# Kernel tuning notes

Measured on AMD Instinct MI355X. Metric: run time of the kernel, lower is better.

The kernel has to match this reference:

```python
import jax, jax.numpy as jnp
import numpy as np

E, T, A, H = 64, 128, 32, 4
S, O, QH1, QD, C1 = 256, 128, 128, 64, 128  # state, obs, query hidden, query/key dim, c hidden


def setup_inputs() -> dict:
    key = jax.random.key(0)
    ks = jax.random.split(key, 10)
    w = 0.02
    return {
        "q_values": jax.random.normal(ks[0], (E, T, A), jnp.float32),
        "states": jax.random.normal(ks[1], (E, T, S), jnp.float32),
        "individual_fs": jax.random.normal(ks[2], (E, T, A, O), jnp.float32),
        "Wq1": jax.random.normal(ks[3], (S, QH1), jnp.float32) * w,
        "bq1": jnp.zeros((QH1,), jnp.float32),
        "Wq2": jax.random.normal(ks[4], (QH1, QD), jnp.float32) * w,
        "bq2": jnp.zeros((QD,), jnp.float32),
        "Wk": jax.random.normal(ks[5], (H, O, QD), jnp.float32) * w,
        "bk": jnp.zeros((H, QD), jnp.float32),
        "Wc1": jax.random.normal(ks[6], (S, C1), jnp.float32) * w,
        "bc1": jnp.zeros((C1,), jnp.float32),
        "Wc2": jax.random.normal(ks[7], (C1, 1), jnp.float32) * w,
        "bc2": jnp.zeros((1,), jnp.float32),
    }


def reference(q_values, states, individual_fs, Wq1, bq1, Wq2, bq2, Wk, bk, Wc1, bc1, Wc2, bc2):
    e, t, a = q_values.shape
    s = states.reshape(-1, states.shape[-1])              # (B, S), B = E*T
    f = individual_fs.reshape(e * t, a, -1)               # (B, A, O)
    # query embedding of state: 2-layer MLP with ReLU
    emb_s = jnp.maximum(s @ Wq1 + bq1, 0.0) @ Wq2 + bq2   # (B, QD)
    # all-agents, all-heads key extraction in one batched einsum
    emb_u = jnp.einsum('bao,hok->bahk', f, Wk) + bk       # (B, A, H, QD)
    # query-key dot products per agent/head, then sum over heads
    Lambda_i = jnp.einsum('bk,bahk->bah', emb_s, emb_u).sum(axis=-1)  # (B, A)
    # state-dependent scalar bias
    c_value = jnp.maximum(s @ Wc1 + bc1, 0.0) @ Wc2 + bc2  # (B, 1)
    Q_tot = jnp.sum(Lambda_i * q_values.reshape(-1, a), axis=-1, keepdims=True) + c_value
    return Q_tot.reshape(e, t, 1)
```

## Files before the change

kernel.cpp:

```cpp
#include <hip/hip_runtime.h>


static constexpr int Sd  = 256;
static constexpr int Ad  = 32;
static constexpr int Od  = 128;
static constexpr int QDd = 64;
static constexpr int NB  = 8;
static constexpr int A_BLOCKS = 1024;
static constexpr int B_BLOCKS = 2048;

__global__ void qatten_prep(const float* __restrict__ Wk, const float* __restrict__ bk,
                            float* __restrict__ WkT, float* __restrict__ bkSum)
{
    int idx = blockIdx.x * 256 + threadIdx.x;
    int k = idx >> 7;
    int o = idx & 127;
    float s = 0.f;
#pragma unroll
    for (int h = 0; h < 4; ++h) s += Wk[h * (Od * QDd) + o * QDd + k];
    WkT[k * Od + o] = s;
    if (idx < QDd) {
        float t = 0.f;
#pragma unroll
        for (int h = 0; h < 4; ++h) t += bk[h * QDd + idx];
        bkSum[idx] = t;
    }
}

__global__ __launch_bounds__(256, 6) void qatten_main(
    const float* __restrict__ qv, const float* __restrict__ st, const float* __restrict__ fs,
    const float* __restrict__ Wq1, const float* __restrict__ bq1,
    const float* __restrict__ Wq2, const float* __restrict__ bq2,
    const float* __restrict__ Wc1, const float* __restrict__ bc1,
    const float* __restrict__ Wc2, const float* __restrict__ bc2,
    const float* __restrict__ WkT, const float* __restrict__ bkSum,
    float* __restrict__ v_out, float* __restrict__ bias_out, float* __restrict__ g_out)
{
    __shared__ float s_lds[NB][Sd];
    __shared__ float h_lds[NB][260];
    __shared__ float emb_lds[NB][QDd];

    const int tid = threadIdx.x;

    if (blockIdx.x < A_BLOCKS) {
        const int b0 = blockIdx.x * NB;

        {
            const float4* sp = (const float4*)(st + (size_t)b0 * Sd);
            float4* sl = (float4*)&s_lds[0][0];
            sl[tid] = sp[tid];
            sl[tid + 256] = sp[tid + 256];
        }
        __syncthreads();

        {
            const float* W  = (tid < 128) ? (Wq1 + tid) : (Wc1 + (tid - 128));
            const float  bb = (tid < 128) ? bq1[tid] : bc1[tid - 128];
            float acc[NB];
#pragma unroll
            for (int r = 0; r < NB; ++r) acc[r] = 0.f;
#pragma unroll 4
            for (int i = 0; i < Sd; i += 4) {
                const float w0 = W[(size_t)(i + 0) * 128];
                const float w1 = W[(size_t)(i + 1) * 128];
                const float w2 = W[(size_t)(i + 2) * 128];
                const float w3 = W[(size_t)(i + 3) * 128];
#pragma unroll
                for (int r = 0; r < NB; ++r) {
                    const float4 sv = *(const float4*)&s_lds[r][i];
                    float a = acc[r];
                    a = fmaf(sv.x, w0, a);
                    a = fmaf(sv.y, w1, a);
                    a = fmaf(sv.z, w2, a);
                    a = fmaf(sv.w, w3, a);
                    acc[r] = a;
                }
            }
#pragma unroll
            for (int r = 0; r < NB; ++r)
                h_lds[r][tid] = fmaxf(acc[r] + bb, 0.f);
        }
        __syncthreads();

        {
            const int k = tid & 63;
            const int rg = tid >> 6;
            float a0 = 0.f, a1 = 0.f;
#pragma unroll 4
            for (int j = 0; j < 128; j += 4) {
                const float w0 = Wq2[(size_t)(j + 0) * 64 + k];
                const float w1 = Wq2[(size_t)(j + 1) * 64 + k];
                const float w2 = Wq2[(size_t)(j + 2) * 64 + k];
                const float w3 = Wq2[(size_t)(j + 3) * 64 + k];
                const float4 h0 = *(const float4*)&h_lds[rg][j];
                const float4 h1 = *(const float4*)&h_lds[rg + 4][j];
                a0 = fmaf(h0.x, w0, a0);  a1 = fmaf(h1.x, w0, a1);
                a0 = fmaf(h0.y, w1, a0);  a1 = fmaf(h1.y, w1, a1);
                a0 = fmaf(h0.z, w2, a0);  a1 = fmaf(h1.z, w2, a1);
                a0 = fmaf(h0.w, w3, a0);  a1 = fmaf(h1.w, w3, a1);
            }
            const float bias = bq2[k];
            emb_lds[rg][k] = a0 + bias;
            emb_lds[rg + 4][k] = a1 + bias;
        }
        __syncthreads();

        {
            const int o = tid & 127;
            const int rg = (tid >> 7) * 4;
            float acc[4] = {0.f, 0.f, 0.f, 0.f};
#pragma unroll 4
            for (int k = 0; k < QDd; k += 4) {
                const float w0 = WkT[(size_t)(k + 0) * 128 + o];
                const float w1 = WkT[(size_t)(k + 1) * 128 + o];
                const float w2 = WkT[(size_t)(k + 2) * 128 + o];
                const float w3 = WkT[(size_t)(k + 3) * 128 + o];
#pragma unroll
                for (int r = 0; r < 4; ++r) {
                    const float4 ev = *(const float4*)&emb_lds[rg + r][k];
                    float a = acc[r];
                    a = fmaf(ev.x, w0, a);
                    a = fmaf(ev.y, w1, a);
                    a = fmaf(ev.z, w2, a);
                    a = fmaf(ev.w, w3, a);
                    acc[r] = a;
                }
            }
#pragma unroll
            for (int r = 0; r < 4; ++r)
                v_out[(size_t)(b0 + rg + r) * Od + o] = acc[r];
        }

        {
            const int b = tid >> 5;
            const int i = tid & 31;
            float pb = 0.f, pc = 0.f;
#pragma unroll
            for (int k = i; k < QDd; k += 32)  pb = fmaf(emb_lds[b][k], bkSum[k], pb);
#pragma unroll
            for (int j = i; j < 128; j += 32)  pc = fmaf(h_lds[b][128 + j], Wc2[j], pc);
            float pq = qv[(size_t)b0 * Ad + tid];
#pragma unroll
            for (int d = 16; d >= 1; d >>= 1) {
                pb += __shfl_down(pb, d, 32);
                pc += __shfl_down(pc, d, 32);
                pq += __shfl_down(pq, d, 32);
            }
            if (i == 0) bias_out[b0 + b] = (pc + bc2[0]) + pb * pq;
        }
    } else {
        const int bb = ((int)blockIdx.x - A_BLOCKS) * 4 + (tid >> 6);
        const int l  = tid & 63;
        const float4* __restrict__ fb = (const float4*)fs + (size_t)bb * (Ad * Od / 4);
        const float qreg = qv[(size_t)bb * Ad + (l & 31)];
        float4 acc = {0.f, 0.f, 0.f, 0.f};
#pragma unroll
        for (int i = 0; i < 16; ++i) {
            const float4 f4 = fb[i * 64 + l];
            const float  qa = __shfl(qreg, 2 * i + (l >> 5), 64);
            acc.x = fmaf(qa, f4.x, acc.x);
            acc.y = fmaf(qa, f4.y, acc.y);
            acc.z = fmaf(qa, f4.z, acc.z);
            acc.w = fmaf(qa, f4.w, acc.w);
        }
        acc.x += __shfl_xor(acc.x, 32, 64);
        acc.y += __shfl_xor(acc.y, 32, 64);
        acc.z += __shfl_xor(acc.z, 32, 64);
        acc.w += __shfl_xor(acc.w, 32, 64);
        if (l < 32)
            *(float4*)(g_out + (size_t)bb * Od + l * 4) = acc;
    }
}

__global__ __launch_bounds__(256, 8) void qatten_final(
    const float* __restrict__ g, const float* __restrict__ v,
    const float* __restrict__ bias, float* __restrict__ out)
{
    const int tid = threadIdx.x;
    const int b = blockIdx.x * 8 + (tid >> 5);
    const int i = tid & 31;
    const float4 gv = *(const float4*)(g + (size_t)b * Od + i * 4);
    const float4 vv = *(const float4*)(v + (size_t)b * Od + i * 4);
    float d = gv.x * vv.x;
    d = fmaf(gv.y, vv.y, d);
    d = fmaf(gv.z, vv.z, d);
    d = fmaf(gv.w, vv.w, d);
#pragma unroll
    for (int k = 16; k >= 1; k >>= 1) d += __shfl_down(d, k, 32);
    if (i == 0) out[b] = d + bias[b];
}

extern "C" void kernel_launch(void* const* d_in, const int* in_sizes, int n_in,
                              void* d_out, int out_size, void* d_ws, size_t ws_size,
                              hipStream_t stream) {
    const float* qv  = (const float*)d_in[0];
    const float* st  = (const float*)d_in[1];
    const float* fs  = (const float*)d_in[2];
    const float* Wq1 = (const float*)d_in[3];
    const float* bq1 = (const float*)d_in[4];
    const float* Wq2 = (const float*)d_in[5];
    const float* bq2 = (const float*)d_in[6];
    const float* Wk  = (const float*)d_in[7];
    const float* bk  = (const float*)d_in[8];
    const float* Wc1 = (const float*)d_in[9];
    const float* bc1 = (const float*)d_in[10];
    const float* Wc2 = (const float*)d_in[11];
    const float* bc2 = (const float*)d_in[12];
    float* out = (float*)d_out;

    float* WkT   = (float*)d_ws;
    float* bkSum = WkT + QDd * Od;
    float* bias  = bkSum + QDd;
    float* vbuf  = bias + 8192;
    float* gbuf  = vbuf + 8192 * Od;

    qatten_prep<<<32, 256, 0, stream>>>(Wk, bk, WkT, bkSum);
    qatten_main<<<A_BLOCKS + B_BLOCKS, 256, 0, stream>>>(
        qv, st, fs, Wq1, bq1, Wq2, bq2, Wc1, bc1, Wc2, bc2,
        WkT, bkSum, vbuf, bias, gbuf);
    qatten_final<<<1024, 256, 0, stream>>>(gbuf, vbuf, bias, out);
}
```

Before: 256.5 us.

## Register-tile MLP GEMMs with 16-row blocks and two rows per wave in gather path

Doubles the rows per block in the state-MLP path to 16 and rewrites the three small GEMMs as 4x4 (or 2x4) register tiles with float4 weight loads. This raises arithmetic reuse per weight load and cuts global weight traffic per row. The feature-gather path now handles two rows per wave so more loads are in flight per thread. Occupancy drops (launch bounds 6 to 4, more LDS per block), and there are half as many blocks.

```diff
diff --git a/kernel.cpp b/kernel.cpp
--- a/kernel.cpp
+++ b/kernel.cpp
@@ -5,9 +5,9 @@
 static constexpr int Ad  = 32;
 static constexpr int Od  = 128;
 static constexpr int QDd = 64;
-static constexpr int NB  = 8;
-static constexpr int A_BLOCKS = 1024;
-static constexpr int B_BLOCKS = 2048;
+static constexpr int NB  = 16;
+static constexpr int A_BLOCKS = 512;
+static constexpr int B_BLOCKS = 1024;
 
 __global__ void qatten_prep(const float* __restrict__ Wk, const float* __restrict__ bk,
                             float* __restrict__ WkT, float* __restrict__ bkSum)
@@ -27,7 +27,7 @@
     }
 }
 
-__global__ __launch_bounds__(256, 6) void qatten_main(
+__global__ __launch_bounds__(256, 4) void qatten_main(
     const float* __restrict__ qv, const float* __restrict__ st, const float* __restrict__ fs,
     const float* __restrict__ Wq1, const float* __restrict__ bq1,
     const float* __restrict__ Wq2, const float* __restrict__ bq2,
@@ -38,7 +38,7 @@
 {
     __shared__ float s_lds[NB][Sd];
     __shared__ float h_lds[NB][260];
-    __shared__ float emb_lds[NB][QDd];
+    __shared__ float emb_lds[NB][68];
 
     const int tid = threadIdx.x;
 
@@ -48,127 +48,174 @@
         {
             const float4* sp = (const float4*)(st + (size_t)b0 * Sd);
             float4* sl = (float4*)&s_lds[0][0];
-            sl[tid] = sp[tid];
+            sl[tid]       = sp[tid];
             sl[tid + 256] = sp[tid + 256];
+            sl[tid + 512] = sp[tid + 512];
+            sl[tid + 768] = sp[tid + 768];
         }
         __syncthreads();
 
         {
-            const float* W  = (tid < 128) ? (Wq1 + tid) : (Wc1 + (tid - 128));
-            const float  bb = (tid < 128) ? bq1[tid] : bc1[tid - 128];
-            float acc[NB];
-#pragma unroll
-            for (int r = 0; r < NB; ++r) acc[r] = 0.f;
-#pragma unroll 4
-            for (int i = 0; i < Sd; i += 4) {
-                const float w0 = W[(size_t)(i + 0) * 128];
-                const float w1 = W[(size_t)(i + 1) * 128];
-                const float w2 = W[(size_t)(i + 2) * 128];
-                const float w3 = W[(size_t)(i + 3) * 128];
-#pragma unroll
-                for (int r = 0; r < NB; ++r) {
-                    const float4 sv = *(const float4*)&s_lds[r][i];
-                    float a = acc[r];
-                    a = fmaf(sv.x, w0, a);
-                    a = fmaf(sv.y, w1, a);
-                    a = fmaf(sv.z, w2, a);
-                    a = fmaf(sv.w, w3, a);
-                    acc[r] = a;
-                }
-            }
-#pragma unroll
-            for (int r = 0; r < NB; ++r)
-                h_lds[r][tid] = fmaxf(acc[r] + bb, 0.f);
+            const int wg = tid & 63;
+            const int rg = (tid >> 6) << 2;
+            const float* __restrict__ Wb = (wg < 32) ? (Wq1 + 4 * wg)
+                                                     : (Wc1 + 4 * (wg - 32));
+            const float4 bb4 = (wg < 32) ? *(const float4*)&bq1[4 * wg]
+                                         : *(const float4*)&bc1[4 * (wg - 32)];
+            float acc[4][4];
+#pragma unroll
+            for (int r = 0; r < 4; ++r)
+#pragma unroll
+                for (int c = 0; c < 4; ++c) acc[r][c] = 0.f;
+
+            for (int k = 0; k < Sd; k += 4) {
+                float w[4][4], sv[4][4];
+#pragma unroll
+                for (int kk = 0; kk < 4; ++kk) {
+                    const float4 t = *(const float4*)&Wb[(size_t)(k + kk) * 128];
+                    w[kk][0] = t.x; w[kk][1] = t.y; w[kk][2] = t.z; w[kk][3] = t.w;
+                }
+#pragma unroll
+                for (int r = 0; r < 4; ++r) {
+                    const float4 t = *(const float4*)&s_lds[rg + r][k];
+                    sv[r][0] = t.x; sv[r][1] = t.y; sv[r][2] = t.z; sv[r][3] = t.w;
+                }
+#pragma unroll
+                for (int r = 0; r < 4; ++r)
+#pragma unroll
+                    for (int kk = 0; kk < 4; ++kk)
+#pragma unroll
+                        for (int c = 0; c < 4; ++c)
+                            acc[r][c] = fmaf(sv[r][kk], w[kk][c], acc[r][c]);
+            }
+#pragma unroll
+            for (int r = 0; r < 4; ++r) {
+                float4 o;
+                o.x = fmaxf(acc[r][0] + bb4.x, 0.f);
+                o.y = fmaxf(acc[r][1] + bb4.y, 0.f);
+                o.z = fmaxf(acc[r][2] + bb4.z, 0.f);
+                o.w = fmaxf(acc[r][3] + bb4.w, 0.f);
+                *(float4*)&h_lds[rg + r][4 * wg] = o;
+            }
         }
         __syncthreads();
 
         {
-            const int k = tid & 63;
-            const int rg = tid >> 6;
-            float a0 = 0.f, a1 = 0.f;
-#pragma unroll 4
-            for (int j = 0; j < 128; j += 4) {
-                const float w0 = Wq2[(size_t)(j + 0) * 64 + k];
-                const float w1 = Wq2[(size_t)(j + 1) * 64 + k];
-                const float w2 = Wq2[(size_t)(j + 2) * 64 + k];
-                const float w3 = Wq2[(size_t)(j + 3) * 64 + k];
-                const float4 h0 = *(const float4*)&h_lds[rg][j];
-                const float4 h1 = *(const float4*)&h_lds[rg + 4][j];
-                a0 = fmaf(h0.x, w0, a0);  a1 = fmaf(h1.x, w0, a1);
-                a0 = fmaf(h0.y, w1, a0);  a1 = fmaf(h1.y, w1, a1);
-                a0 = fmaf(h0.z, w2, a0);  a1 = fmaf(h1.z, w2, a1);
-                a0 = fmaf(h0.w, w3, a0);  a1 = fmaf(h1.w, w3, a1);
-            }
-            const float bias = bq2[k];
-            emb_lds[rg][k] = a0 + bias;
-            emb_lds[rg + 4][k] = a1 + bias;
+            const int cg = tid & 15;
+            const int row = tid >> 4;
+            float acc[4] = {0.f, 0.f, 0.f, 0.f};
+            for (int k = 0; k < 128; k += 4) {
+                float w[4][4];
+#pragma unroll
+                for (int kk = 0; kk < 4; ++kk) {
+                    const float4 t = *(const float4*)&Wq2[(size_t)(k + kk) * 64 + 4 * cg];
+                    w[kk][0] = t.x; w[kk][1] = t.y; w[kk][2] = t.z; w[kk][3] = t.w;
+                }
+                const float4 h4 = *(const float4*)&h_lds[row][k];
+                float hv[4] = {h4.x, h4.y, h4.z, h4.w};
+#pragma unroll
+                for (int kk = 0; kk < 4; ++kk)
+#pragma unroll
+                    for (int c = 0; c < 4; ++c)
+                        acc[c] = fmaf(hv[kk], w[kk][c], acc[c]);
+            }
+            const float4 b4 = *(const float4*)&bq2[4 * cg];
+            float4 o;
+            o.x = acc[0] + b4.x; o.y = acc[1] + b4.y;
+            o.z = acc[2] + b4.z; o.w = acc[3] + b4.w;
+            *(float4*)&emb_lds[row][4 * cg] = o;
         }
         __syncthreads();
 
         {
-            const int o = tid & 127;
-            const int rg = (tid >> 7) * 4;
-            float acc[4] = {0.f, 0.f, 0.f, 0.f};
-#pragma unroll 4
+            const int cg = tid & 31;
+            const int rp = (tid >> 5) << 1;
+            float acc[2][4];
+#pragma unroll
+            for (int r = 0; r < 2; ++r)
+#pragma unroll
+                for (int c = 0; c < 4; ++c) acc[r][c] = 0.f;
             for (int k = 0; k < QDd; k += 4) {
-                const float w0 = WkT[(size_t)(k + 0) * 128 + o];
-                const float w1 = WkT[(size_t)(k + 1) * 128 + o];
-                const float w2 = WkT[(size_t)(k + 2) * 128 + o];
-                const float w3 = WkT[(size_t)(k + 3) * 128 + o];
-#pragma unroll
-                for (int r = 0; r < 4; ++r) {
-                    const float4 ev = *(const float4*)&emb_lds[rg + r][k];
-                    float a = acc[r];
-                    a = fmaf(ev.x, w0, a);
-                    a = fmaf(ev.y, w1, a);
-                    a = fmaf(ev.z, w2, a);
-                    a = fmaf(ev.w, w3, a);
-                    acc[r] = a;
-                }
-            }
-#pragma unroll
-            for (int r = 0; r < 4; ++r)
-                v_out[(size_t)(b0 + rg + r) * Od + o] = acc[r];
-        }
-
-        {
-            const int b = tid >> 5;
-            const int i = tid & 31;
+                float w[4][4], ev[2][4];
+#pragma unroll
+                for (int kk = 0; kk < 4; ++kk) {
+                    const float4 t = *(const float4*)&WkT[(size_t)(k + kk) * 128 + 4 * cg];
+                    w[kk][0] = t.x; w[kk][1] = t.y; w[kk][2] = t.z; w[kk][3] = t.w;
+                }
+#pragma unroll
+                for (int r = 0; r < 2; ++r) {
+                    const float4 t = *(const float4*)&emb_lds[rp + r][k];
+                    ev[r][0] = t.x; ev[r][1] = t.y; ev[r][2] = t.z; ev[r][3] = t.w;
+                }
+#pragma unroll
+                for (int r = 0; r < 2; ++r)
+#pragma unroll
+                    for (int kk = 0; kk < 4; ++kk)
+#pragma unroll
+                        for (int c = 0; c < 4; ++c)
+                            acc[r][c] = fmaf(ev[r][kk], w[kk][c], acc[r][c]);
+            }
+#pragma unroll
+            for (int r = 0; r < 2; ++r) {
+                float4 o;
+                o.x = acc[r][0]; o.y = acc[r][1]; o.z = acc[r][2]; o.w = acc[r][3];
+                *(float4*)&v_out[(size_t)(b0 + rp + r) * Od + 4 * cg] = o;
+            }
+        }
+
+        {
+            const int b = tid >> 4;
+            const int i = tid & 15;
             float pb = 0.f, pc = 0.f;
 #pragma unroll
-            for (int k = i; k < QDd; k += 32)  pb = fmaf(emb_lds[b][k], bkSum[k], pb);
-#pragma unroll
-            for (int j = i; j < 128; j += 32)  pc = fmaf(h_lds[b][128 + j], Wc2[j], pc);
-            float pq = qv[(size_t)b0 * Ad + tid];
-#pragma unroll
-            for (int d = 16; d >= 1; d >>= 1) {
-                pb += __shfl_down(pb, d, 32);
-                pc += __shfl_down(pc, d, 32);
-                pq += __shfl_down(pq, d, 32);
+            for (int k = i; k < QDd; k += 16)  pb = fmaf(emb_lds[b][k], bkSum[k], pb);
+#pragma unroll
+            for (int j = i; j < 128; j += 16)  pc = fmaf(h_lds[b][128 + j], Wc2[j], pc);
+            float pq = qv[(size_t)(b0 + b) * Ad + i] + qv[(size_t)(b0 + b) * Ad + i + 16];
+#pragma unroll
+            for (int d = 8; d >= 1; d >>= 1) {
+                pb += __shfl_down(pb, d, 16);
+                pc += __shfl_down(pc, d, 16);
+                pq += __shfl_down(pq, d, 16);
             }
             if (i == 0) bias_out[b0 + b] = (pc + bc2[0]) + pb * pq;
         }
     } else {
-        const int bb = ((int)blockIdx.x - A_BLOCKS) * 4 + (tid >> 6);
-        const int l  = tid & 63;
-        const float4* __restrict__ fb = (const float4*)fs + (size_t)bb * (Ad * Od / 4);
-        const float qreg = qv[(size_t)bb * Ad + (l & 31)];
-        float4 acc = {0.f, 0.f, 0.f, 0.f};
+        const int w = tid >> 6;
+        const int l = tid & 63;
+        const int r0 = ((int)blockIdx.x - A_BLOCKS) * 8 + w * 2;
+        const float4* __restrict__ f0 = (const float4*)fs + (size_t)r0 * (Ad * Od / 4);
+        const float4* __restrict__ f1 = f0 + (Ad * Od / 4);
+        const float q0 = qv[(size_t)r0 * Ad + (l & 31)];
+        const float q1 = qv[(size_t)(r0 + 1) * Ad + (l & 31)];
+        float4 a0 = {0.f, 0.f, 0.f, 0.f}, a1 = {0.f, 0.f, 0.f, 0.f};
 #pragma unroll
         for (int i = 0; i < 16; ++i) {
-            const float4 f4 = fb[i * 64 + l];
-            const float  qa = __shfl(qreg, 2 * i + (l >> 5), 64);
-            acc.x = fmaf(qa, f4.x, acc.x);
-            acc.y = fmaf(qa, f4.y, acc.y);
-            acc.z = fmaf(qa, f4.z, acc.z);
-            acc.w = fmaf(qa, f4.w, acc.w);
-        }
-        acc.x += __shfl_xor(acc.x, 32, 64);
-        acc.y += __shfl_xor(acc.y, 32, 64);
-        acc.z += __shfl_xor(acc.z, 32, 64);
-        acc.w += __shfl_xor(acc.w, 32, 64);
-        if (l < 32)
-            *(float4*)(g_out + (size_t)bb * Od + l * 4) = acc;
+            const float4 x0 = f0[i * 64 + l];
+            const float4 x1 = f1[i * 64 + l];
+            const float qa0 = __shfl(q0, 2 * i + (l >> 5), 64);
+            const float qa1 = __shfl(q1, 2 * i + (l >> 5), 64);
+            a0.x = fmaf(qa0, x0.x, a0.x);
+            a0.y = fmaf(qa0, x0.y, a0.y);
+            a0.z = fmaf(qa0, x0.z, a0.z);
+            a0.w = fmaf(qa0, x0.w, a0.w);
+            a1.x = fmaf(qa1, x1.x, a1.x);
+            a1.y = fmaf(qa1, x1.y, a1.y);
+            a1.z = fmaf(qa1, x1.z, a1.z);
+            a1.w = fmaf(qa1, x1.w, a1.w);
+        }
+        a0.x += __shfl_xor(a0.x, 32, 64);
+        a0.y += __shfl_xor(a0.y, 32, 64);
+        a0.z += __shfl_xor(a0.z, 32, 64);
+        a0.w += __shfl_xor(a0.w, 32, 64);
+        a1.x += __shfl_xor(a1.x, 32, 64);
+        a1.y += __shfl_xor(a1.y, 32, 64);
+        a1.z += __shfl_xor(a1.z, 32, 64);
+        a1.w += __shfl_xor(a1.w, 32, 64);
+        if (l < 32) {
+            *(float4*)(g_out + (size_t)r0 * Od + l * 4) = a0;
+            *(float4*)(g_out + (size_t)(r0 + 1) * Od + l * 4) = a1;
+        }
     }
 }
 
```

After: 242.8 us. 5.3% less time.
